# Optimization experiments

Measured on AMD Instinct MI355X. Metric: run time of the kernel, lower is better.

## Reference

```python
import jax, jax.numpy as jnp
import numpy as np

N0, N1, N2, N3 = 1982464, 123904, 11264, 1024
E0, E1, E2 = 1858560, 112640, 10240
D_IN, D_H, D_OUT = 128, 256, 47


def setup_inputs() -> dict:
    key = jax.random.key(0)
    ks = jax.random.split(key, 16)
    inp = {
        "x": jax.random.normal(ks[0], (N0, D_IN), jnp.float32),
        "Wl0": jax.random.normal(ks[1], (D_IN, D_H), jnp.float32) * (1.0 / np.sqrt(D_IN)),
        "Wr0": jax.random.normal(ks[2], (D_IN, D_H), jnp.float32) * (1.0 / np.sqrt(D_IN)),
        "b0": jnp.zeros((D_H,), jnp.float32),
        "Wl1": jax.random.normal(ks[3], (D_H, D_H), jnp.float32) * (1.0 / np.sqrt(D_H)),
        "Wr1": jax.random.normal(ks[4], (D_H, D_H), jnp.float32) * (1.0 / np.sqrt(D_H)),
        "b1": jnp.zeros((D_H,), jnp.float32),
        "Wl2": jax.random.normal(ks[5], (D_H, D_OUT), jnp.float32) * (1.0 / np.sqrt(D_H)),
        "Wr2": jax.random.normal(ks[6], (D_H, D_OUT), jnp.float32) * (1.0 / np.sqrt(D_H)),
        "b2": jnp.zeros((D_OUT,), jnp.float32),
        "src0": jax.random.randint(ks[7], (E0,), 0, N0, jnp.int64 if jax.config.jax_enable_x64 else jnp.int32),
        "dst0": jax.random.randint(ks[8], (E0,), 0, N1, jnp.int32),
        "src1": jax.random.randint(ks[9], (E1,), 0, N1, jnp.int32),
        "dst1": jax.random.randint(ks[10], (E1,), 0, N2, jnp.int32),
        "src2": jax.random.randint(ks[11], (E2,), 0, N2, jnp.int32),
        "dst2": jax.random.randint(ks[12], (E2,), 0, N3, jnp.int32),
        "n1": N1,
        "n2": N2,
        "n3": N3,
    }
    return inp


def _sage_conv(x, src, dst, n_tgt, Wl, Wr, b):
    # PyG SAGEConv (mean aggr, bipartite): out = lin_l(mean_j x_src[j]) + lin_r(x_tgt)
    msgs = x[src]  # [E, d] irregular gather
    agg = jax.ops.segment_sum(msgs, dst, num_segments=n_tgt)
    cnt = jax.ops.segment_sum(jnp.ones((src.shape[0],), x.dtype), dst, num_segments=n_tgt)
    agg = agg / jnp.maximum(cnt, 1.0)[:, None]
    return agg @ Wl + x[:n_tgt] @ Wr + b


def reference(x, Wl0, Wr0, b0, Wl1, Wr1, b1, Wl2, Wr2, b2,
              src0, dst0, src1, dst1, src2, dst2, n1, n2, n3):
    # Layer 0 -> relu (dropout is identity in eval mode)
    h = jax.nn.relu(_sage_conv(x, src0, dst0, n1, Wl0, Wr0, b0))
    # Layer 1 -> relu
    h = jax.nn.relu(_sage_conv(h, src1, dst1, n2, Wl1, Wr1, b1))
    # Layer 2 -> log_softmax
    h = _sage_conv(h, src2, dst2, n3, Wl2, Wr2, b2)
    return jax.nn.log_softmax(h, axis=-1)
```

## Files before the change

kernel.cpp:

```cpp
#include <hip/hip_runtime.h>
#include <cstdint>
#include <cstddef>

#define N0C 1982464
#define N1C 123904
#define N2C 11264
#define N3C 1024

__global__ __launch_bounds__(256) void hist_k(const int* __restrict__ dst, int* __restrict__ cnt, int E) {
    int i = blockIdx.x * 256 + threadIdx.x;
    if (i < E) atomicAdd(&cnt[dst[i]], 1);
}

__global__ __launch_bounds__(256) void scan1_k(const int* __restrict__ in, int* __restrict__ out,
                                               int* __restrict__ bsum, int n) {
    __shared__ int sd[256];
    int t = threadIdx.x;
    int base = blockIdx.x * 1024 + t * 4;
    int v0 = (base + 0 < n) ? in[base + 0] : 0;
    int v1 = (base + 1 < n) ? in[base + 1] : 0;
    int v2 = (base + 2 < n) ? in[base + 2] : 0;
    int v3 = (base + 3 < n) ? in[base + 3] : 0;
    sd[t] = v0 + v1 + v2 + v3;
    __syncthreads();
    for (int off = 1; off < 256; off <<= 1) {
        int tmp = 0;
        if (t >= off) tmp = sd[t - off];
        __syncthreads();
        if (t >= off) sd[t] += tmp;
        __syncthreads();
    }
    int run = (t > 0) ? sd[t - 1] : 0;
    if (base + 0 < n) out[base + 0] = run; run += v0;
    if (base + 1 < n) out[base + 1] = run; run += v1;
    if (base + 2 < n) out[base + 2] = run; run += v2;
    if (base + 3 < n) out[base + 3] = run;
    if (t == 255) bsum[blockIdx.x] = sd[255];
}

__global__ __launch_bounds__(256) void scan2_k(int* bsum, int nb) {
    __shared__ int sd[256];
    int t = threadIdx.x;
    sd[t] = (t < nb) ? bsum[t] : 0;
    __syncthreads();
    for (int off = 1; off < 256; off <<= 1) {
        int tmp = 0;
        if (t >= off) tmp = sd[t - off];
        __syncthreads();
        if (t >= off) sd[t] += tmp;
        __syncthreads();
    }
    if (t < nb) bsum[t] = (t > 0) ? sd[t - 1] : 0;
}

__global__ __launch_bounds__(256) void scanadd_k(int* __restrict__ out, const int* __restrict__ bsum,
                                                 int n, int E) {
    int i = blockIdx.x * 256 + threadIdx.x;
    if (i < n) out[i] += bsum[i >> 10];
    if (i == 0) out[n] = E;
}

__global__ __launch_bounds__(256) void scatter_k(const int* __restrict__ src, const int* __restrict__ dst,
                                                 const int* __restrict__ rowoff, int* __restrict__ cursor,
                                                 int* __restrict__ perm, int E) {
    int i = blockIdx.x * 256 + threadIdx.x;
    if (i < E) {
        int d = dst[i];
        int p = atomicAdd(&cursor[d], 1);
        perm[rowoff[d] + p] = src[i];
    }
}

template<int VEC>
__global__ __launch_bounds__(256) void aggregate_k(const float* __restrict__ x, const int* __restrict__ perm,
                                                   const int* __restrict__ rowoff, float* __restrict__ agg,
                                                   int n) {
    int node = (int)((blockIdx.x * 256 + threadIdx.x) >> 6);
    int lane = threadIdx.x & 63;
    if (node >= n) return;
    int beg = rowoff[node], end = rowoff[node + 1];
    float a0 = 0.f, a1 = 0.f, a2 = 0.f, a3 = 0.f;
    for (int e = beg; e < end; ++e) {
        int s = perm[e];
        if constexpr (VEC == 2) {
            const float2* row = (const float2*)(x + (size_t)s * 128);
            float2 r = row[lane];
            a0 += r.x; a1 += r.y;
        } else {
            const float4* row = (const float4*)(x + (size_t)s * 256);
            float4 r = row[lane];
            a0 += r.x; a1 += r.y; a2 += r.z; a3 += r.w;
        }
    }
    int c = end - beg;
    float inv = (c > 0) ? 1.0f / (float)c : 0.0f;
    if constexpr (VEC == 2) {
        float2* o = (float2*)(agg + (size_t)node * 128);
        o[lane] = make_float2(a0 * inv, a1 * inv);
    } else {
        float4* o = (float4*)(agg + (size_t)node * 256);
        o[lane] = make_float4(a0 * inv, a1 * inv, a2 * inv, a3 * inv);
    }
}

template<bool RELU>
__global__ __launch_bounds__(256) void gemm2_k(const float* __restrict__ A1, const float* __restrict__ A2,
                                               const float* __restrict__ W1, const float* __restrict__ W2,
                                               const float* __restrict__ bias, float* __restrict__ C,
                                               int M, int N, int K) {
    __shared__ float As[16][68];
    __shared__ float Bs[16][68];
    int row0 = blockIdx.x * 64;
    int col0 = blockIdx.y * 64;
    int t = threadIdx.x;
    int tx = t & 15, ty = t >> 4;
    float acc[4][4] = {};
    bool colsFull = (col0 + 64 <= N) && ((N & 3) == 0);
    for (int p = 0; p < 2; ++p) {
        const float* A = p ? A2 : A1;
        const float* W = p ? W2 : W1;
        for (int k0 = 0; k0 < K; k0 += 16) {
            {
                int r = t >> 2, c4 = (t & 3) * 4;
                float4 av = *(const float4*)(A + (size_t)(row0 + r) * K + k0 + c4);
                As[c4 + 0][r] = av.x;
                As[c4 + 1][r] = av.y;
                As[c4 + 2][r] = av.z;
                As[c4 + 3][r] = av.w;
            }
            if (colsFull) {
                int r = t >> 4, c4 = (t & 15) * 4;
                float4 wv = *(const float4*)(W + (size_t)(k0 + r) * N + col0 + c4);
                *(float4*)&Bs[r][c4] = wv;
            } else {
                #pragma unroll
                for (int i = 0; i < 4; ++i) {
                    int l = t + i * 256;
                    int r = l >> 6, c = l & 63;
                    int col = col0 + c;
                    Bs[r][c] = (col < N) ? W[(size_t)(k0 + r) * N + col] : 0.0f;
                }
            }
            __syncthreads();
            #pragma unroll
            for (int k = 0; k < 16; ++k) {
                float4 av = *(const float4*)&As[k][ty * 4];
                float4 bv = *(const float4*)&Bs[k][tx * 4];
                float a[4] = {av.x, av.y, av.z, av.w};
                float b[4] = {bv.x, bv.y, bv.z, bv.w};
                #pragma unroll
                for (int i = 0; i < 4; ++i)
                    #pragma unroll
                    for (int j = 0; j < 4; ++j)
                        acc[i][j] += a[i] * b[j];
            }
            __syncthreads();
        }
    }
    #pragma unroll
    for (int i = 0; i < 4; ++i) {
        int r = row0 + ty * 4 + i;
        #pragma unroll
        for (int j = 0; j < 4; ++j) {
            int col = col0 + tx * 4 + j;
            if (r < M && col < N) {
                float v = acc[i][j] + bias[col];
                if (RELU) v = fmaxf(v, 0.0f);
                C[(size_t)r * N + col] = v;
            }
        }
    }
}

__global__ __launch_bounds__(256) void logsoftmax_k(float* __restrict__ io, int M, int N) {
    int w = (int)((blockIdx.x * 256 + threadIdx.x) >> 6);
    int lane = threadIdx.x & 63;
    if (w >= M) return;
    float v = (lane < N) ? io[(size_t)w * N + lane] : -1e30f;
    float m = v;
    for (int off = 32; off > 0; off >>= 1) m = fmaxf(m, __shfl_xor(m, off));
    float e = (lane < N) ? expf(v - m) : 0.0f;
    float s = e;
    for (int off = 32; off > 0; off >>= 1) s += __shfl_xor(s, off);
    float r = v - m - logf(s);
    if (lane < N) io[(size_t)w * N + lane] = r;
}

extern "C" void kernel_launch(void* const* d_in, const int* in_sizes, int n_in,
                              void* d_out, int out_size, void* d_ws, size_t ws_size,
                              hipStream_t stream) {
    const float* x   = (const float*)d_in[0];
    const float* Wl0 = (const float*)d_in[1];
    const float* Wr0 = (const float*)d_in[2];
    const float* b0  = (const float*)d_in[3];
    const float* Wl1 = (const float*)d_in[4];
    const float* Wr1 = (const float*)d_in[5];
    const float* b1  = (const float*)d_in[6];
    const float* Wl2 = (const float*)d_in[7];
    const float* Wr2 = (const float*)d_in[8];
    const float* b2  = (const float*)d_in[9];
    const int* src0  = (const int*)d_in[10];
    const int* dst0  = (const int*)d_in[11];
    const int* src1  = (const int*)d_in[12];
    const int* dst1  = (const int*)d_in[13];
    const int* src2  = (const int*)d_in[14];
    const int* dst2  = (const int*)d_in[15];
    const int E0 = in_sizes[10], E1 = in_sizes[12], E2 = in_sizes[14];
    float* out = (float*)d_out;

    char* w = (char*)d_ws;
    auto alloc = [&](size_t bytes) { char* p = w; w += (bytes + 255) & ~(size_t)255; return p; };
    float* agg0 = (float*)alloc((size_t)N1C * 128 * 4);
    float* h1   = (float*)alloc((size_t)N1C * 256 * 4);
    float* agg1 = (float*)alloc((size_t)N2C * 256 * 4);
    float* h2   = (float*)alloc((size_t)N2C * 256 * 4);
    float* agg2 = (float*)alloc((size_t)N3C * 256 * 4);
    int* zreg = (int*)alloc((size_t)2 * (N1C + N2C + N3C) * 4);
    int* cnt0 = zreg;           int* cur0 = cnt0 + N1C;
    int* cnt1 = cur0 + N1C;     int* cur1 = cnt1 + N2C;
    int* cnt2 = cur1 + N2C;     int* cur2 = cnt2 + N3C;
    int* ro0   = (int*)alloc((size_t)(N1C + 1) * 4);
    int* ro1   = (int*)alloc((size_t)(N2C + 1) * 4);
    int* ro2   = (int*)alloc((size_t)(N3C + 1) * 4);
    int* perm0 = (int*)alloc((size_t)E0 * 4);
    int* perm1 = (int*)alloc((size_t)E1 * 4);
    int* perm2 = (int*)alloc((size_t)E2 * 4);
    int* bsum  = (int*)alloc(256 * 4);

    hipMemsetAsync(zreg, 0, (size_t)2 * (N1C + N2C + N3C) * 4, stream);

    auto csr = [&](const int* srcA, const int* dstA, int E, int n,
                   int* cnt, int* cur, int* ro, int* perm) {
        hist_k<<<dim3((E + 255) / 256), dim3(256), 0, stream>>>(dstA, cnt, E);
        int nb = (n + 1023) / 1024;
        scan1_k<<<dim3(nb), dim3(256), 0, stream>>>(cnt, ro, bsum, n);
        scan2_k<<<dim3(1), dim3(256), 0, stream>>>(bsum, nb);
        scanadd_k<<<dim3((n + 255) / 256), dim3(256), 0, stream>>>(ro, bsum, n, E);
        scatter_k<<<dim3((E + 255) / 256), dim3(256), 0, stream>>>(srcA, dstA, ro, cur, perm, E);
    };

    csr(src0, dst0, E0, N1C, cnt0, cur0, ro0, perm0);
    aggregate_k<2><<<dim3((N1C + 3) / 4), dim3(256), 0, stream>>>(x, perm0, ro0, agg0, N1C);
    gemm2_k<true><<<dim3(N1C / 64, 4), dim3(256), 0, stream>>>(agg0, x, Wl0, Wr0, b0, h1, N1C, 256, 128);

    csr(src1, dst1, E1, N2C, cnt1, cur1, ro1, perm1);
    aggregate_k<4><<<dim3((N2C + 3) / 4), dim3(256), 0, stream>>>(h1, perm1, ro1, agg1, N2C);
    gemm2_k<true><<<dim3(N2C / 64, 4), dim3(256), 0, stream>>>(agg1, h1, Wl1, Wr1, b1, h2, N2C, 256, 256);

    csr(src2, dst2, E2, N3C, cnt2, cur2, ro2, perm2);
    aggregate_k<4><<<dim3((N3C + 3) / 4), dim3(256), 0, stream>>>(h2, perm2, ro2, agg2, N3C);
    gemm2_k<false><<<dim3(N3C / 64, 1), dim3(256), 0, stream>>>(agg2, h2, Wl2, Wr2, b2, out, N3C, 47, 256);
    logsoftmax_k<<<dim3((N3C + 3) / 4), dim3(256), 0, stream>>>(out, N3C, 47);
}
```

Before: 1.966 ms.

## Use bf16 MFMA GEMMs for layers 0-1 and store intermediates in bf16

Replaces the fp32 SIMT GEMM for the first two SAGE layers with a bf16 MFMA kernel that computes all 256 output columns per block, using pre-transposed bf16 weights. The aggregated features, the x[:n1] slice and the layer-1 hidden state are kept in bf16, which halves their memory traffic, including the irregular gather in layer 1. It adds cast kernels for x and the weights on every call and lowers precision, which may change accuracy relative to the fp32 reference.

```diff
diff --git a/kernel.cpp b/kernel.cpp
--- a/kernel.cpp
+++ b/kernel.cpp
@@ -6,6 +6,18 @@
 #define N1C 123904
 #define N2C 11264
 #define N3C 1024
+
+typedef __attribute__((ext_vector_type(8))) short bf16x8;
+typedef __attribute__((ext_vector_type(4))) float f32x4;
+
+__device__ __forceinline__ unsigned short f2b(float f) {
+    unsigned u = __float_as_uint(f);
+    unsigned r = (u + 0x7FFFu + ((u >> 16) & 1u)) >> 16;
+    return (unsigned short)r;
+}
+__device__ __forceinline__ float b2f(unsigned short h) {
+    return __uint_as_float(((unsigned)h) << 16);
+}
 
 __global__ __launch_bounds__(256) void hist_k(const int* __restrict__ dst, int* __restrict__ cnt, int E) {
     int i = blockIdx.x * 256 + threadIdx.x;
@@ -71,35 +83,125 @@
     }
 }
 
-template<int VEC>
-__global__ __launch_bounds__(256) void aggregate_k(const float* __restrict__ x, const int* __restrict__ perm,
-                                                   const int* __restrict__ rowoff, float* __restrict__ agg,
-                                                   int n) {
+__global__ __launch_bounds__(256) void castx_k(const float* __restrict__ x, unsigned short* __restrict__ xb,
+                                               int n4) {
+    int i = blockIdx.x * 256 + threadIdx.x;
+    if (i < n4) {
+        float4 v = ((const float4*)x)[i];
+        ((ushort4*)xb)[i] = make_ushort4(f2b(v.x), f2b(v.y), f2b(v.z), f2b(v.w));
+    }
+}
+
+__global__ __launch_bounds__(256) void castwt_k(const float* __restrict__ W, unsigned short* __restrict__ Wt,
+                                                int K, int N) {
+    int i = blockIdx.x * 256 + threadIdx.x;
+    if (i < N * K) {
+        int n = i / K, k = i - n * K;
+        Wt[i] = f2b(W[(size_t)k * N + n]);
+    }
+}
+
+__global__ __launch_bounds__(256) void agg0_k(const float* __restrict__ x, const int* __restrict__ perm,
+                                              const int* __restrict__ ro, unsigned short* __restrict__ agg,
+                                              int n) {
     int node = (int)((blockIdx.x * 256 + threadIdx.x) >> 6);
     int lane = threadIdx.x & 63;
     if (node >= n) return;
-    int beg = rowoff[node], end = rowoff[node + 1];
+    int beg = ro[node], end = ro[node + 1];
+    float a0 = 0.f, a1 = 0.f;
+    for (int e = beg; e < end; ++e) {
+        int s = perm[e];
+        float2 r = ((const float2*)(x + (size_t)s * 128))[lane];
+        a0 += r.x; a1 += r.y;
+    }
+    float inv = (end > beg) ? 1.0f / (float)(end - beg) : 0.0f;
+    unsigned pack = (unsigned)f2b(a0 * inv) | ((unsigned)f2b(a1 * inv) << 16);
+    ((unsigned*)(agg + (size_t)node * 128))[lane] = pack;
+}
+
+__global__ __launch_bounds__(256) void agg1_k(const unsigned short* __restrict__ h, const int* __restrict__ perm,
+                                              const int* __restrict__ ro, unsigned short* __restrict__ agg,
+                                              int n) {
+    int node = (int)((blockIdx.x * 256 + threadIdx.x) >> 6);
+    int lane = threadIdx.x & 63;
+    if (node >= n) return;
+    int beg = ro[node], end = ro[node + 1];
     float a0 = 0.f, a1 = 0.f, a2 = 0.f, a3 = 0.f;
     for (int e = beg; e < end; ++e) {
         int s = perm[e];
-        if constexpr (VEC == 2) {
-            const float2* row = (const float2*)(x + (size_t)s * 128);
-            float2 r = row[lane];
-            a0 += r.x; a1 += r.y;
-        } else {
-            const float4* row = (const float4*)(x + (size_t)s * 256);
-            float4 r = row[lane];
-            a0 += r.x; a1 += r.y; a2 += r.z; a3 += r.w;
+        ushort4 r = ((const ushort4*)(h + (size_t)s * 256))[lane];
+        a0 += b2f(r.x); a1 += b2f(r.y); a2 += b2f(r.z); a3 += b2f(r.w);
+    }
+    float inv = (end > beg) ? 1.0f / (float)(end - beg) : 0.0f;
+    ((ushort4*)(agg + (size_t)node * 256))[lane] =
+        make_ushort4(f2b(a0 * inv), f2b(a1 * inv), f2b(a2 * inv), f2b(a3 * inv));
+}
+
+__global__ __launch_bounds__(256) void agg2_k(const float* __restrict__ x, const int* __restrict__ perm,
+                                              const int* __restrict__ ro, float* __restrict__ agg, int n) {
+    int node = (int)((blockIdx.x * 256 + threadIdx.x) >> 6);
+    int lane = threadIdx.x & 63;
+    if (node >= n) return;
+    int beg = ro[node], end = ro[node + 1];
+    float a0 = 0.f, a1 = 0.f, a2 = 0.f, a3 = 0.f;
+    for (int e = beg; e < end; ++e) {
+        int s = perm[e];
+        float4 r = ((const float4*)(x + (size_t)s * 256))[lane];
+        a0 += r.x; a1 += r.y; a2 += r.z; a3 += r.w;
+    }
+    float inv = (end > beg) ? 1.0f / (float)(end - beg) : 0.0f;
+    ((float4*)(agg + (size_t)node * 256))[lane] = make_float4(a0 * inv, a1 * inv, a2 * inv, a3 * inv);
+}
+
+template<bool RELU, bool OUTBF16>
+__global__ __launch_bounds__(256) void gemm_mfma_k(
+    const unsigned short* __restrict__ A1, const unsigned short* __restrict__ A2,
+    const unsigned short* __restrict__ Wt1, const unsigned short* __restrict__ Wt2,
+    const float* __restrict__ bias, void* __restrict__ Cout, int M, int K) {
+    __shared__ short As[64][40];
+    __shared__ short Bs[256][40];
+    const int t = threadIdx.x;
+    const int row0 = blockIdx.x * 64;
+    const int wv = t >> 6, lane = t & 63;
+    const int m16 = lane & 15, quad = lane >> 4;
+    f32x4 acc[16] = {};
+    for (int p = 0; p < 2; ++p) {
+        const unsigned short* A  = p ? A2 : A1;
+        const unsigned short* Wt = p ? Wt2 : Wt1;
+        for (int k0 = 0; k0 < K; k0 += 32) {
+            {
+                int r = t >> 2, kc = (t & 3) * 8;
+                *(int4*)&As[r][kc] = *(const int4*)(A + (size_t)(row0 + r) * K + k0 + kc);
+            }
+            {
+                const unsigned short* src = Wt + (size_t)t * K + k0;
+                *(int4*)&Bs[t][0]  = *(const int4*)(src + 0);
+                *(int4*)&Bs[t][8]  = *(const int4*)(src + 8);
+                *(int4*)&Bs[t][16] = *(const int4*)(src + 16);
+                *(int4*)&Bs[t][24] = *(const int4*)(src + 24);
+            }
+            __syncthreads();
+            bf16x8 a = *(const bf16x8*)&As[wv * 16 + m16][quad * 8];
+            #pragma unroll
+            for (int c = 0; c < 16; ++c) {
+                bf16x8 b = *(const bf16x8*)&Bs[c * 16 + m16][quad * 8];
+                acc[c] = __builtin_amdgcn_mfma_f32_16x16x32_bf16(a, b, acc[c], 0, 0, 0);
+            }
+            __syncthreads();
         }
     }
-    int c = end - beg;
-    float inv = (c > 0) ? 1.0f / (float)c : 0.0f;
-    if constexpr (VEC == 2) {
-        float2* o = (float2*)(agg + (size_t)node * 128);
-        o[lane] = make_float2(a0 * inv, a1 * inv);
-    } else {
-        float4* o = (float4*)(agg + (size_t)node * 256);
-        o[lane] = make_float4(a0 * inv, a1 * inv, a2 * inv, a3 * inv);
+    #pragma unroll
+    for (int c = 0; c < 16; ++c) {
+        int col = c * 16 + m16;
+        float bv = bias[col];
+        #pragma unroll
+        for (int f = 0; f < 4; ++f) {
+            int row = row0 + wv * 16 + quad * 4 + f;
+            float v = acc[c][f] + bv;
+            if (RELU) v = fmaxf(v, 0.0f);
+            if (OUTBF16) ((unsigned short*)Cout)[(size_t)row * 256 + col] = f2b(v);
+            else         ((float*)Cout)[(size_t)row * 256 + col] = v;
+        }
     }
 }
 
@@ -210,11 +312,16 @@
 
     char* w = (char*)d_ws;
     auto alloc = [&](size_t bytes) { char* p = w; w += (bytes + 255) & ~(size_t)255; return p; };
-    float* agg0 = (float*)alloc((size_t)N1C * 128 * 4);
-    float* h1   = (float*)alloc((size_t)N1C * 256 * 4);
-    float* agg1 = (float*)alloc((size_t)N2C * 256 * 4);
+    unsigned short* agg0 = (unsigned short*)alloc((size_t)N1C * 128 * 2);
+    unsigned short* xb   = (unsigned short*)alloc((size_t)N1C * 128 * 2);
+    unsigned short* h1   = (unsigned short*)alloc((size_t)N1C * 256 * 2);
+    unsigned short* agg1 = (unsigned short*)alloc((size_t)N2C * 256 * 2);
     float* h2   = (float*)alloc((size_t)N2C * 256 * 4);
     float* agg2 = (float*)alloc((size_t)N3C * 256 * 4);
+    unsigned short* Wt0l = (unsigned short*)alloc((size_t)256 * 128 * 2);
+    unsigned short* Wt0r = (unsigned short*)alloc((size_t)256 * 128 * 2);
+    unsigned short* Wt1l = (unsigned short*)alloc((size_t)256 * 256 * 2);
+    unsigned short* Wt1r = (unsigned short*)alloc((size_t)256 * 256 * 2);
     int* zreg = (int*)alloc((size_t)2 * (N1C + N2C + N3C) * 4);
     int* cnt0 = zreg;           int* cur0 = cnt0 + N1C;
     int* cnt1 = cur0 + N1C;     int* cur1 = cnt1 + N2C;
@@ -239,16 +346,22 @@
         scatter_k<<<dim3((E + 255) / 256), dim3(256), 0, stream>>>(srcA, dstA, ro, cur, perm, E);
     };
 
+    castwt_k<<<dim3((256 * 128 + 255) / 256), dim3(256), 0, stream>>>(Wl0, Wt0l, 128, 256);
+    castwt_k<<<dim3((256 * 128 + 255) / 256), dim3(256), 0, stream>>>(Wr0, Wt0r, 128, 256);
+    castwt_k<<<dim3((256 * 256 + 255) / 256), dim3(256), 0, stream>>>(Wl1, Wt1l, 256, 256);
+    castwt_k<<<dim3((256 * 256 + 255) / 256), dim3(256), 0, stream>>>(Wr1, Wt1r, 256, 256);
+    castx_k<<<dim3((N1C * 128 / 4 + 255) / 256), dim3(256), 0, stream>>>(x, xb, N1C * 128 / 4);
+
     csr(src0, dst0, E0, N1C, cnt0, cur0, ro0, perm0);
-    aggregate_k<2><<<dim3((N1C + 3) / 4), dim3(256), 0, stream>>>(x, perm0, ro0, agg0, N1C);
-    gemm2_k<true><<<dim3(N1C / 64, 4), dim3(256), 0, stream>>>(agg0, x, Wl0, Wr0, b0, h1, N1C, 256, 128);
+    agg0_k<<<dim3((N1C + 3) / 4), dim3(256), 0, stream>>>(x, perm0, ro0, agg0, N1C);
+    gemm_mfma_k<true, true><<<dim3(N1C / 64), dim3(256), 0, stream>>>(agg0, xb, Wt0l, Wt0r, b0, h1, N1C, 128);
 
     csr(src1, dst1, E1, N2C, cnt1, cur1, ro1, perm1);
-    aggregate_k<4><<<dim3((N2C + 3) / 4), dim3(256), 0, stream>>>(h1, perm1, ro1, agg1, N2C);
-    gemm2_k<true><<<dim3(N2C / 64, 4), dim3(256), 0, stream>>>(agg1, h1, Wl1, Wr1, b1, h2, N2C, 256, 256);
+    agg1_k<<<dim3((N2C + 3) / 4), dim3(256), 0, stream>>>(h1, perm1, ro1, agg1, N2C);
+    gemm_mfma_k<true, false><<<dim3(N2C / 64), dim3(256), 0, stream>>>(agg1, h1, Wt1l, Wt1r, b1, h2, N2C, 256);
 
     csr(src2, dst2, E2, N3C, cnt2, cur2, ro2, perm2);
-    aggregate_k<4><<<dim3((N3C + 3) / 4), dim3(256), 0, stream>>>(h2, perm2, ro2, agg2, N3C);
+    agg2_k<<<dim3((N3C + 3) / 4), dim3(256), 0, stream>>>(h2, perm2, ro2, agg2, N3C);
     gemm2_k<false><<<dim3(N3C / 64, 1), dim3(256), 0, stream>>>(agg2, h2, Wl2, Wr2, b2, out, N3C, 47, 256);
     logsoftmax_k<<<dim3((N3C + 3) / 4), dim3(256), 0, stream>>>(out, N3C, 47);
 }
```

After: 1.780 ms. 9.4% less time.
